# Kernel tuning notes

Hardware: AMD Instinct MI355X
Metric: run time of the kernel (lower is better)

## Reference

```python
import jax, jax.numpy as jnp
import numpy as np


def setup_inputs() -> dict:
    key = jax.random.key(0)
    ks = jax.random.split(key, 5)
    B, D, L, NH = 2, 1024, 2048, 8
    H = D // NH  # number of SSM heads / filter channels
    return {
        "v": jax.random.normal(ks[0], (B, D, L), jnp.float32),
        "k": jax.random.normal(ks[1], (H, L), jnp.float32) * 0.1,
        "bias": jax.random.normal(ks[2], (D,), jnp.float32),
        "x1": jax.random.normal(ks[3], (B, D, L), jnp.float32),
        "x2": jax.random.normal(ks[4], (B, D, L), jnp.float32),
        "num_heads": NH,
    }


def reference(v, k, bias, x1, x2, num_heads):
    # Multi-head Hyena FFT long conv with fused gating (safari fftconv_h3 semantics):
    #   kv[b,h,d1,d2,l] = v[b,h,d1,l] * x2[b,h,d2,l]
    #   y = causal_fftconv(kv, k[h]) + bias[h,d1] * kv
    #   out[b,h,d2,l] = sum_d1 y[b,h,d1,d2,l] * x1[b,h,d1,l]
    B, D, L = v.shape
    H = D // num_heads
    fft_size = 2 * L  # zero-pad to 2L for linear (causal) convolution
    vr = v.reshape(B, H, num_heads, L)
    x1r = x1.reshape(B, H, num_heads, L)
    x2r = x2.reshape(B, H, num_heads, L)
    kv = vr[:, :, :, None, :] * x2r[:, :, None, :, :]  # (B, H, d1, d2, L)
    k_f = jnp.fft.rfft(k.astype(jnp.float32), n=fft_size)  # (H, fft_size//2+1)
    y = jnp.fft.irfft(
        jnp.fft.rfft(kv, n=fft_size) * k_f[None, :, None, None, :], n=fft_size
    )[..., :L]  # (B, H, d1, d2, L)
    skip = bias.astype(jnp.float32).reshape(H, num_heads)[None, :, :, None, None]
    y = y + kv * skip
    out = jnp.einsum("bhijl,bhil->bhjl", y, x1r)  # contract d1 with q-gate
    return out.reshape(B, D, L)
```

## Files before the change

kernel.cpp:

```cpp
#include <hip/hip_runtime.h>
#include <stdint.h>


typedef __attribute__((ext_vector_type(8))) short bf16x8;
typedef __attribute__((ext_vector_type(4))) float f32x4;
typedef __attribute__((ext_vector_type(2))) float f32x2;

#define NHd  8
#define SC   128
#define GW   192

static __device__ __forceinline__ uint32_t pkbf(float a, float b) {
    const uint32_t ua = __float_as_uint(a) + 0x8000u;
    const uint32_t ub = __float_as_uint(b) + 0x8000u;
    return __builtin_amdgcn_perm(ub, ua, 0x07060302u);
}

static __device__ __forceinline__ uint32_t pktr(f32x2 p) {
    union { f32x2 f; uint32_t u[2]; } c; c.f = p;
    return __builtin_amdgcn_perm(c.u[1], c.u[0], 0x07060302u);
}

static __device__ __forceinline__ uint32_t gmul2(f32x2 s, f32x2 g) {
    return pktr(s * g);
}

union U8 { uint32_t u[4]; bf16x8 v; uint4 q; };

__global__ __launch_bounds__(256, 6) void hyena_mfma9_kernel(
    const float* __restrict__ v, const float* __restrict__ kf,
    const float* __restrict__ bias, const float* __restrict__ x1,
    const float* __restrict__ x2, float* __restrict__ out,
    int B, int H, int L)
{
    __shared__ __align__(16) float  ks[2048];
    __shared__ __align__(16) float4 gwin[GW];
    __shared__ __align__(16) ushort vT[2][SC][NHd];
    __shared__ __align__(16) ushort x2T[2][NHd][136];
    __shared__ float sbuf[2][64];

    const int tid  = threadIdx.x;
    const int h    = blockIdx.x;
    const int l0b  = ((int)gridDim.y - 1 - (int)blockIdx.y) * 64;
    const int nk   = l0b + 64;

    const int lane = tid & 63, wv = tid >> 6;
    const int lq   = lane & 15, quad = lane >> 4;
    const int wb   = wv >> 1;
    const int wl0  = l0b + (wv & 1) * 32;
    const int baseb = (wb * H + h) * NHd * L;

    for (int i = tid; i < nk; i += 256) ks[i] = kf[h * L + i];

    bf16x8 xf0 = {}, xf1 = {};
    if (quad == 0) {
        float a0[NHd], a1[NHd];
#pragma unroll
        for (int d1 = 0; d1 < NHd; ++d1) {
            a0[d1] = x1[baseb + d1 * L + wl0 + lq];
            a1[d1] = x1[baseb + d1 * L + wl0 + 16 + lq];
        }
        U8 u0, u1;
#pragma unroll
        for (int j = 0; j < 4; ++j) {
            u0.u[j] = pkbf(a0[2 * j], a0[2 * j + 1]);
            u1.u[j] = pkbf(a1[2 * j], a1[2 * j + 1]);
        }
        xf0 = u0.v; xf1 = u1.v;
    }

    if (tid < 128) {
        const int bb = tid >> 6, l = tid & 63;
        const int bs = (bb * H + h) * NHd * L;
        float s = 0.f;
#pragma unroll
        for (int d1 = 0; d1 < NHd; ++d1)
            s += bias[h * NHd + d1] * x1[bs + d1 * L + l0b + l]
                                    * v [bs + d1 * L + l0b + l];
        sbuf[bb][l] = s;
    }

    f32x4 acc0 = {0.f, 0.f, 0.f, 0.f}, acc1 = {0.f, 0.f, 0.f, 0.f};
    const int wlmax = wl0 + 31;
    const int ebase = 127 + (wv & 1) * 32 + lq - 4 * quad;

    bool gfirst = true;
    float4 g10c = {0.f, 0.f, 0.f, 0.f};

    for (int s0 = 0; s0 < nk; s0 += SC) {
        __syncthreads();
        {
            const int bb = tid >> 7, row = tid & 127;
            const int bs = (bb * H + h) * NHd * L;
            const float* vp = v + bs + s0 + row;
            float f[NHd];
#pragma unroll
            for (int d1 = 0; d1 < NHd; ++d1) f[d1] = vp[d1 * L];
            *(uint4*)&vT[bb][row][0] = make_uint4(
                pkbf(f[0], f[1]), pkbf(f[2], f[3]),
                pkbf(f[4], f[5]), pkbf(f[6], f[7]));

            const int d2 = row >> 4, ms = (row & 15) * 8;
            const int G = ms & ~31;
            const int o = ms & 31;
            const int pa = ((o >> 2) & 3) * 8 + (o >> 4) * 4;
            const float* xp = x2 + bs + d2 * L + s0 + ms;
            const float4 q0 = *(const float4*)xp;
            const float4 q1 = *(const float4*)(xp + 4);
            *(uint2*)&x2T[bb][d2][G + pa] =
                make_uint2(pkbf(q0.x, q0.y), pkbf(q0.z, q0.w));
            *(uint2*)&x2T[bb][d2][G + pa + 8] =
                make_uint2(pkbf(q1.x, q1.y), pkbf(q1.z, q1.w));
        }
        if (tid < GW - 1) {
            const int i = l0b - s0 - 127 + tid;
            float4 w = {0.f, 0.f, 0.f, 0.f};
            if (i >= 3) {
                w.x = ks[i]; w.y = ks[i - 1]; w.z = ks[i - 2]; w.w = ks[i - 3];
            } else if (i >= 0) {
                w.x = ks[i];
                if (i >= 1) w.y = ks[i - 1];
                if (i >= 2) w.z = ks[i - 2];
            }
            gwin[tid] = w;
        }
        __syncthreads();

        const int cmax = min(SC, wlmax - s0 + 1);
        for (int c = 0; c < cmax; c += 32) {
            bf16x8 av0 = {}, av1 = {};
            if (quad == 0) {
                av0 = *(const bf16x8*)&vT[wb][c + lq][0];
                av1 = *(const bf16x8*)&vT[wb][c + 16 + lq][0];
            }
            const int ge = ebase - c;
            float4 g10;
            if (gfirst) { g10 = *(const float4*)&gwin[ge + 16]; gfirst = false; }
            else        g10 = g10c;
            const float4 g00 = *(const float4*)&gwin[ge];
            const float4 g01 = *(const float4*)&gwin[ge - 16];
            g10c = g01;
            const bf16x8 ax = *(const bf16x8*)&x2T[wb][lq & 7][c + 8 * quad];

            const f32x4 Z = {0.f, 0.f, 0.f, 0.f};
            const f32x4 S00 = __builtin_amdgcn_mfma_f32_16x16x32_bf16(av0, xf0, Z, 0, 0, 0);
            const f32x4 S01 = __builtin_amdgcn_mfma_f32_16x16x32_bf16(av1, xf0, Z, 0, 0, 0);
            const f32x4 S10 = __builtin_amdgcn_mfma_f32_16x16x32_bf16(av0, xf1, Z, 0, 0, 0);
            const f32x4 S11 = __builtin_amdgcn_mfma_f32_16x16x32_bf16(av1, xf1, Z, 0, 0, 0);

            U8 p0, p1;
            p0.u[0] = gmul2((f32x2){S00[0], S00[1]}, (f32x2){g00.x, g00.y});
            p0.u[1] = gmul2((f32x2){S00[2], S00[3]}, (f32x2){g00.z, g00.w});
            p0.u[2] = gmul2((f32x2){S01[0], S01[1]}, (f32x2){g01.x, g01.y});
            p0.u[3] = gmul2((f32x2){S01[2], S01[3]}, (f32x2){g01.z, g01.w});
            p1.u[0] = gmul2((f32x2){S10[0], S10[1]}, (f32x2){g10.x, g10.y});
            p1.u[1] = gmul2((f32x2){S10[2], S10[3]}, (f32x2){g10.z, g10.w});
            p1.u[2] = gmul2((f32x2){S11[0], S11[1]}, (f32x2){g00.x, g00.y});
            p1.u[3] = gmul2((f32x2){S11[2], S11[3]}, (f32x2){g00.z, g00.w});

            acc0 = __builtin_amdgcn_mfma_f32_16x16x32_bf16(ax, p0.v, acc0, 0, 0, 0);
            acc1 = __builtin_amdgcn_mfma_f32_16x16x32_bf16(ax, p1.v, acc1, 0, 0, 0);
        }
    }

    if (quad < 2) {
        const int d2b = 4 * quad;
        const int lA  = wl0 + lq;
        const float sb0 = sbuf[wb][(wv & 1) * 32 + lq];
        const float sb1 = sbuf[wb][(wv & 1) * 32 + 16 + lq];
#pragma unroll
        for (int r = 0; r < 4; ++r) {
            const int ro = baseb + (d2b + r) * L + lA;
            out[ro]      = acc0[r] + x2[ro]      * sb0;
            out[ro + 16] = acc1[r] + x2[ro + 16] * sb1;
        }
    }
}

extern "C" void kernel_launch(void* const* d_in, const int* in_sizes, int n_in,
                              void* d_out, int out_size, void* d_ws, size_t ws_size,
                              hipStream_t stream) {
    const float* v    = (const float*)d_in[0];
    const float* k    = (const float*)d_in[1];
    const float* bias = (const float*)d_in[2];
    const float* x1   = (const float*)d_in[3];
    const float* x2   = (const float*)d_in[4];
    float* out = (float*)d_out;

    const int D = in_sizes[2];
    const int H = D / NHd;
    const int L = in_sizes[1] / H;
    const int B = in_sizes[0] / (D * L);

    dim3 grid(H, L / 64);
    hyena_mfma9_kernel<<<grid, 256, 0, stream>>>(v, k, bias, x1, x2, out, B, H, L);
}
```

Before: 153.5 us.

## Widen output tile to 128 positions per block with four accumulators per wave

Each block now covers 128 output positions instead of 64, and each wave computes 64 positions using four MFMA accumulators. Each vT/x2T chunk staged in shared memory is therefore reused across twice as many outputs, which halves the redundant staging of v/x2 and the gwin setup across blocks. A rolling five-register window of Toeplitz kernel values is reused between iterations. The cost is more registers (launch bounds drop from 6 to 5 blocks), half as many blocks, and a larger causal triangle imbalance per block.

```diff
diff --git a/kernel.cpp b/kernel.cpp
--- a/kernel.cpp
+++ b/kernel.cpp
@@ -8,7 +8,7 @@
 
 #define NHd  8
 #define SC   128
-#define GW   192
+#define GW   256
 
 static __device__ __forceinline__ uint32_t pkbf(float a, float b) {
     const uint32_t ua = __float_as_uint(a) + 0x8000u;
@@ -27,7 +27,7 @@
 
 union U8 { uint32_t u[4]; bf16x8 v; uint4 q; };
 
-__global__ __launch_bounds__(256, 6) void hyena_mfma9_kernel(
+__global__ __launch_bounds__(256, 5) void hyena_mfma10_kernel(
     const float* __restrict__ v, const float* __restrict__ kf,
     const float* __restrict__ bias, const float* __restrict__ x1,
     const float* __restrict__ x2, float* __restrict__ out,
@@ -37,40 +37,39 @@
     __shared__ __align__(16) float4 gwin[GW];
     __shared__ __align__(16) ushort vT[2][SC][NHd];
     __shared__ __align__(16) ushort x2T[2][NHd][136];
-    __shared__ float sbuf[2][64];
+    __shared__ float sbuf[2][128];
 
     const int tid  = threadIdx.x;
     const int h    = blockIdx.x;
-    const int l0b  = ((int)gridDim.y - 1 - (int)blockIdx.y) * 64;
-    const int nk   = l0b + 64;
+    const int l0b  = ((int)gridDim.y - 1 - (int)blockIdx.y) * 128;
+    const int nk   = l0b + 128;
 
     const int lane = tid & 63, wv = tid >> 6;
     const int lq   = lane & 15, quad = lane >> 4;
-    const int wb   = wv >> 1;
-    const int wl0  = l0b + (wv & 1) * 32;
+    const int wb   = wv & 1;
+    const int wseg = wv >> 1;
+    const int wl0  = l0b + wseg * 64;
     const int baseb = (wb * H + h) * NHd * L;
 
     for (int i = tid; i < nk; i += 256) ks[i] = kf[h * L + i];
 
-    bf16x8 xf0 = {}, xf1 = {};
+    bf16x8 xf[4] = {};
     if (quad == 0) {
-        float a0[NHd], a1[NHd];
-#pragma unroll
-        for (int d1 = 0; d1 < NHd; ++d1) {
-            a0[d1] = x1[baseb + d1 * L + wl0 + lq];
-            a1[d1] = x1[baseb + d1 * L + wl0 + 16 + lq];
-        }
-        U8 u0, u1;
 #pragma unroll
         for (int j = 0; j < 4; ++j) {
-            u0.u[j] = pkbf(a0[2 * j], a0[2 * j + 1]);
-            u1.u[j] = pkbf(a1[2 * j], a1[2 * j + 1]);
-        }
-        xf0 = u0.v; xf1 = u1.v;
-    }
-
-    if (tid < 128) {
-        const int bb = tid >> 6, l = tid & 63;
+            float a0[NHd];
+#pragma unroll
+            for (int d1 = 0; d1 < NHd; ++d1)
+                a0[d1] = x1[baseb + d1 * L + wl0 + 16 * j + lq];
+            U8 u0;
+#pragma unroll
+            for (int t = 0; t < 4; ++t) u0.u[t] = pkbf(a0[2 * t], a0[2 * t + 1]);
+            xf[j] = u0.v;
+        }
+    }
+
+    {
+        const int bb = tid >> 7, l = tid & 127;
         const int bs = (bb * H + h) * NHd * L;
         float s = 0.f;
 #pragma unroll
@@ -80,12 +79,15 @@
         sbuf[bb][l] = s;
     }
 
-    f32x4 acc0 = {0.f, 0.f, 0.f, 0.f}, acc1 = {0.f, 0.f, 0.f, 0.f};
-    const int wlmax = wl0 + 31;
-    const int ebase = 127 + (wv & 1) * 32 + lq - 4 * quad;
+    f32x4 acc[4];
+#pragma unroll
+    for (int j = 0; j < 4; ++j) acc[j] = (f32x4){0.f, 0.f, 0.f, 0.f};
+
+    const int wlmax = wl0 + 63;
+    const int ebase = 127 + wseg * 64 + lq - 4 * quad;
 
     bool gfirst = true;
-    float4 g10c = {0.f, 0.f, 0.f, 0.f};
+    float4 g0, g1, g2, g3, g4;
 
     for (int s0 = 0; s0 < nk; s0 += SC) {
         __syncthreads();
@@ -128,51 +130,71 @@
 
         const int cmax = min(SC, wlmax - s0 + 1);
         for (int c = 0; c < cmax; c += 32) {
+            const int e = ebase - c;
+
             bf16x8 av0 = {}, av1 = {};
             if (quad == 0) {
                 av0 = *(const bf16x8*)&vT[wb][c + lq][0];
                 av1 = *(const bf16x8*)&vT[wb][c + 16 + lq][0];
             }
-            const int ge = ebase - c;
-            float4 g10;
-            if (gfirst) { g10 = *(const float4*)&gwin[ge + 16]; gfirst = false; }
-            else        g10 = g10c;
-            const float4 g00 = *(const float4*)&gwin[ge];
-            const float4 g01 = *(const float4*)&gwin[ge - 16];
-            g10c = g01;
+            if (gfirst) {
+                g4 = *(const float4*)&gwin[e + 48];
+                g3 = *(const float4*)&gwin[e + 32];
+                g2 = *(const float4*)&gwin[e + 16];
+                gfirst = false;
+            } else { g4 = g2; g3 = g1; g2 = g0; }
+            g1 = *(const float4*)&gwin[e];
+            g0 = *(const float4*)&gwin[e - 16];
             const bf16x8 ax = *(const bf16x8*)&x2T[wb][lq & 7][c + 8 * quad];
 
             const f32x4 Z = {0.f, 0.f, 0.f, 0.f};
-            const f32x4 S00 = __builtin_amdgcn_mfma_f32_16x16x32_bf16(av0, xf0, Z, 0, 0, 0);
-            const f32x4 S01 = __builtin_amdgcn_mfma_f32_16x16x32_bf16(av1, xf0, Z, 0, 0, 0);
-            const f32x4 S10 = __builtin_amdgcn_mfma_f32_16x16x32_bf16(av0, xf1, Z, 0, 0, 0);
-            const f32x4 S11 = __builtin_amdgcn_mfma_f32_16x16x32_bf16(av1, xf1, Z, 0, 0, 0);
-
-            U8 p0, p1;
-            p0.u[0] = gmul2((f32x2){S00[0], S00[1]}, (f32x2){g00.x, g00.y});
-            p0.u[1] = gmul2((f32x2){S00[2], S00[3]}, (f32x2){g00.z, g00.w});
-            p0.u[2] = gmul2((f32x2){S01[0], S01[1]}, (f32x2){g01.x, g01.y});
-            p0.u[3] = gmul2((f32x2){S01[2], S01[3]}, (f32x2){g01.z, g01.w});
-            p1.u[0] = gmul2((f32x2){S10[0], S10[1]}, (f32x2){g10.x, g10.y});
-            p1.u[1] = gmul2((f32x2){S10[2], S10[3]}, (f32x2){g10.z, g10.w});
-            p1.u[2] = gmul2((f32x2){S11[0], S11[1]}, (f32x2){g00.x, g00.y});
-            p1.u[3] = gmul2((f32x2){S11[2], S11[3]}, (f32x2){g00.z, g00.w});
-
-            acc0 = __builtin_amdgcn_mfma_f32_16x16x32_bf16(ax, p0.v, acc0, 0, 0, 0);
-            acc1 = __builtin_amdgcn_mfma_f32_16x16x32_bf16(ax, p1.v, acc1, 0, 0, 0);
+            {
+                const f32x4 Sa0 = __builtin_amdgcn_mfma_f32_16x16x32_bf16(av0, xf[0], Z, 0, 0, 0);
+                const f32x4 Sa1 = __builtin_amdgcn_mfma_f32_16x16x32_bf16(av1, xf[0], Z, 0, 0, 0);
+                const f32x4 Sb0 = __builtin_amdgcn_mfma_f32_16x16x32_bf16(av0, xf[1], Z, 0, 0, 0);
+                const f32x4 Sb1 = __builtin_amdgcn_mfma_f32_16x16x32_bf16(av1, xf[1], Z, 0, 0, 0);
+                U8 p;
+                p.u[0] = gmul2((f32x2){Sa0[0], Sa0[1]}, (f32x2){g1.x, g1.y});
+                p.u[1] = gmul2((f32x2){Sa0[2], Sa0[3]}, (f32x2){g1.z, g1.w});
+                p.u[2] = gmul2((f32x2){Sa1[0], Sa1[1]}, (f32x2){g0.x, g0.y});
+                p.u[3] = gmul2((f32x2){Sa1[2], Sa1[3]}, (f32x2){g0.z, g0.w});
+                acc[0] = __builtin_amdgcn_mfma_f32_16x16x32_bf16(ax, p.v, acc[0], 0, 0, 0);
+                p.u[0] = gmul2((f32x2){Sb0[0], Sb0[1]}, (f32x2){g2.x, g2.y});
+                p.u[1] = gmul2((f32x2){Sb0[2], Sb0[3]}, (f32x2){g2.z, g2.w});
+                p.u[2] = gmul2((f32x2){Sb1[0], Sb1[1]}, (f32x2){g1.x, g1.y});
+                p.u[3] = gmul2((f32x2){Sb1[2], Sb1[3]}, (f32x2){g1.z, g1.w});
+                acc[1] = __builtin_amdgcn_mfma_f32_16x16x32_bf16(ax, p.v, acc[1], 0, 0, 0);
+            }
+            {
+                const f32x4 Sc0 = __builtin_amdgcn_mfma_f32_16x16x32_bf16(av0, xf[2], Z, 0, 0, 0);
+                const f32x4 Sc1 = __builtin_amdgcn_mfma_f32_16x16x32_bf16(av1, xf[2], Z, 0, 0, 0);
+                const f32x4 Sd0 = __builtin_amdgcn_mfma_f32_16x16x32_bf16(av0, xf[3], Z, 0, 0, 0);
+                const f32x4 Sd1 = __builtin_amdgcn_mfma_f32_16x16x32_bf16(av1, xf[3], Z, 0, 0, 0);
+                U8 p;
+                p.u[0] = gmul2((f32x2){Sc0[0], Sc0[1]}, (f32x2){g3.x, g3.y});
+                p.u[1] = gmul2((f32x2){Sc0[2], Sc0[3]}, (f32x2){g3.z, g3.w});
+                p.u[2] = gmul2((f32x2){Sc1[0], Sc1[1]}, (f32x2){g2.x, g2.y});
+                p.u[3] = gmul2((f32x2){Sc1[2], Sc1[3]}, (f32x2){g2.z, g2.w});
+                acc[2] = __builtin_amdgcn_mfma_f32_16x16x32_bf16(ax, p.v, acc[2], 0, 0, 0);
+                p.u[0] = gmul2((f32x2){Sd0[0], Sd0[1]}, (f32x2){g4.x, g4.y});
+                p.u[1] = gmul2((f32x2){Sd0[2], Sd0[3]}, (f32x2){g4.z, g4.w});
+                p.u[2] = gmul2((f32x2){Sd1[0], Sd1[1]}, (f32x2){g3.x, g3.y});
+                p.u[3] = gmul2((f32x2){Sd1[2], Sd1[3]}, (f32x2){g3.z, g3.w});
+                acc[3] = __builtin_amdgcn_mfma_f32_16x16x32_bf16(ax, p.v, acc[3], 0, 0, 0);
+            }
         }
     }
 
     if (quad < 2) {
-        const int d2b = 4 * quad;
-        const int lA  = wl0 + lq;
-        const float sb0 = sbuf[wb][(wv & 1) * 32 + lq];
-        const float sb1 = sbuf[wb][(wv & 1) * 32 + 16 + lq];
-#pragma unroll
-        for (int r = 0; r < 4; ++r) {
-            const int ro = baseb + (d2b + r) * L + lA;
-            out[ro]      = acc0[r] + x2[ro]      * sb0;
-            out[ro + 16] = acc1[r] + x2[ro + 16] * sb1;
+#pragma unroll
+        for (int j = 0; j < 4; ++j) {
+            const int lA  = wl0 + 16 * j + lq;
+            const float sb = sbuf[wb][wseg * 64 + 16 * j + lq];
+#pragma unroll
+            for (int r = 0; r < 4; ++r) {
+                const int ro = baseb + (4 * quad + r) * L + lA;
+                out[ro] = acc[j][r] + x2[ro] * sb;
+            }
         }
     }
 }
@@ -192,6 +214,6 @@
     const int L = in_sizes[1] / H;
     const int B = in_sizes[0] / (D * L);
 
-    dim3 grid(H, L / 64);
-    hyena_mfma9_kernel<<<grid, 256, 0, stream>>>(v, k, bias, x1, x2, out, B, H, L);
-}
+    dim3 grid(H, L / 128);
+    hyena_mfma10_kernel<<<grid, 256, 0, stream>>>(v, k, bias, x1, x2, out, B, H, L);
+}
```

Result: no change. 151.5 us (-1.3%).
